# Optimization experiments

Hardware: AMD Instinct MI355X
Metric: run time of the kernel (lower is better)

Reference implementation:

```python
import jax, jax.numpy as jnp
import numpy as np

DIM = 384
HEADS = 12
WS = 7
HID = 4 * 256  # FFN hidden is hard-coded default 1024, NOT 4*dim
EPS = 1e-5


def layernorm(x, g, b):
    mu = jnp.mean(x, axis=-1, keepdims=True)
    var = jnp.mean(jnp.square(x - mu), axis=-1, keepdims=True)
    return (x - mu) * jax.lax.rsqrt(var + EPS) * g + b


def setup_inputs() -> dict:
    key = jax.random.key(0)
    ks = jax.random.split(key, 12)
    s = 0.02
    return {
        "x": jax.random.normal(ks[0], (32, DIM, 56, 56), dtype=jnp.float32),
        "ln1_g": jnp.ones((DIM,), jnp.float32),
        "ln1_b": jnp.zeros((DIM,), jnp.float32),
        "qkv_w": jax.random.normal(ks[1], (3 * DIM, DIM), jnp.float32) * s,
        "qkv_b": jnp.zeros((3 * DIM,), jnp.float32),
        "proj_w": jax.random.normal(ks[2], (DIM, DIM), jnp.float32) * s,
        "proj_b": jnp.zeros((DIM,), jnp.float32),
        "ln2_g": jnp.ones((DIM,), jnp.float32),
        "ln2_b": jnp.zeros((DIM,), jnp.float32),
        "fc1_w": jax.random.normal(ks[3], (HID, DIM), jnp.float32) * s,
        "fc1_b": jnp.zeros((HID,), jnp.float32),
        "fc2_w": jax.random.normal(ks[4], (DIM, HID), jnp.float32) * s,
        "fc2_b": jnp.zeros((DIM,), jnp.float32),
    }


def window_attention(x, qkv_w, qkv_b, proj_w, proj_b):
    # x: [B, H, W, C] channels-last
    B, H, W, C = x.shape
    Wh, Ww = H // WS, W // WS
    # partition: [B*Wh*Ww, WS*WS, C]
    w = x.reshape(B, Wh, WS, Ww, WS, C).transpose(0, 1, 3, 2, 4, 5)
    w = w.reshape(B * Wh * Ww, WS * WS, C)
    Bn, N, _ = w.shape
    hd = C // HEADS
    qkv = w @ qkv_w.T + qkv_b  # [Bn, N, 3C]
    qkv = qkv.reshape(Bn, N, 3, HEADS, hd).transpose(2, 0, 3, 1, 4)
    q, k, v = qkv[0], qkv[1], qkv[2]  # each [Bn, h, N, hd]
    attn = jnp.einsum('bhnd,bhmd->bhnm', q, k) * (hd ** -0.5)
    attn = jax.nn.softmax(attn, axis=-1)
    o = jnp.einsum('bhnm,bhmd->bhnd', attn, v)
    o = o.transpose(0, 2, 1, 3).reshape(Bn, N, C)
    o = o @ proj_w.T + proj_b
    # reverse
    o = o.reshape(B, Wh, Ww, WS, WS, C).transpose(0, 1, 3, 2, 4, 5)
    return o.reshape(B, H, W, C)


def reference(x, ln1_g, ln1_b, qkv_w, qkv_b, proj_w, proj_b,
              ln2_g, ln2_b, fc1_w, fc1_b, fc2_w, fc2_b):
    # x: [B, C, H, W]
    residual = x
    h = x.transpose(0, 2, 3, 1)  # [B,H,W,C]
    h = layernorm(h, ln1_g, ln1_b)
    h = window_attention(h, qkv_w, qkv_b, proj_w, proj_b)
    x = h.transpose(0, 3, 1, 2) + residual
    residual = x
    h = x.transpose(0, 2, 3, 1)
    h = layernorm(h, ln2_g, ln2_b)
    h = jax.nn.gelu(h @ fc1_w.T + fc1_b, approximate=False)
    h = h @ fc2_w.T + fc2_b
    return h.transpose(0, 3, 1, 2) + residual
```

## Files before the change

### kernel.cpp

```cpp
#include <hip/hip_runtime.h>
#include <cstdint>
#include <cmath>

#define DIM 384
#define HEADS 12
#define TOKENS 100352
#define HW_ 3136
#define NWIN 2048

typedef __attribute__((ext_vector_type(8))) short short8;
typedef __attribute__((ext_vector_type(4))) short short4v;
typedef __attribute__((ext_vector_type(2))) short short2v;
typedef __attribute__((ext_vector_type(4))) float f32x4;

#define AS1 __attribute__((address_space(1)))
#define AS3 __attribute__((address_space(3)))

__device__ __forceinline__ short f2b(float f){
  unsigned u = __builtin_bit_cast(unsigned, f);
  u += 0x7FFFu + ((u >> 16) & 1u);
  return (short)(u >> 16);
}
__device__ __forceinline__ float b2f(short h){
  unsigned u = ((unsigned)(unsigned short)h) << 16;
  return __builtin_bit_cast(float, u);
}

__device__ __forceinline__ void gload_lds16(const short* g, short* l){
  __builtin_amdgcn_global_load_lds((AS1 void*)(g), (AS3 void*)(l), 16, 0, 0);
}

__device__ __forceinline__ float gelu_f(float v){
  float z  = v * 0.70710678118654752f;
  float az = fabsf(z);
  float t  = __builtin_amdgcn_rcpf(1.f + 0.3275911f*az);
  float poly = t*(0.254829592f + t*(-0.284496736f + t*(1.421413741f +
               t*(-1.453152027f + t*1.061405429f))));
  float e  = __expf(-z*z);
  float er = copysignf(1.f - poly*e, z);
  return 0.5f * v * (1.f + er);
}

__global__ void k_cvt(const float* __restrict__ s, short* __restrict__ d, int n){
  int i = blockIdx.x*256 + threadIdx.x;
  if (i < n) d[i] = f2b(s[i]);
}

__global__ __launch_bounds__(256) void k_ln1(const float* __restrict__ x,
    const float* __restrict__ gam, const float* __restrict__ bet,
    short* __restrict__ ln1, short* __restrict__ xr)
{
  __shared__ float red0[256];
  __shared__ float red1[256];
  __shared__ float mus[64], rss[64];
  __shared__ short xfull[64*388];
  int t = threadIdx.x;
  int blk = blockIdx.x;
  int b = blk / 49;
  int hw0 = (blk % 49) * 64;
  int p = t & 63, cq = t >> 6;
  const float* xb = x + (long)b*DIM*HW_ + hw0 + p;
  float s = 0.f, sq = 0.f;
  for (int i = 0; i < 96; i++){
    int c = i*4 + cq;
    float v = xb[(long)c*HW_];
    s += v; sq += v*v;
    xfull[p*388 + c] = f2b(v);
  }
  red0[t] = s; red1[t] = sq;
  __syncthreads();
  if (t < 64){
    float ts = red0[t] + red0[t+64] + red0[t+128] + red0[t+192];
    float tq = red1[t] + red1[t+64] + red1[t+128] + red1[t+192];
    float mu = ts * (1.f/DIM);
    float var = tq * (1.f/DIM) - mu*mu;
    mus[t] = mu;
    rss[t] = rsqrtf(var + 1e-5f);
  }
  __syncthreads();
  int p2 = t >> 2, q4 = t & 3;
  float mu = mus[p2], rs = rss[p2];
  int hwp2 = hw0 + p2;
  int h2 = hwp2 / 56, w2 = hwp2 % 56;
  int wt2 = ((b*8 + h2/7)*8 + w2/7)*49 + (h2%7)*7 + (w2%7);
  long lnbase = (long)wt2*DIM;
  long xrbase = (long)(b*HW_ + hwp2)*DIM;
  #pragma unroll
  for (int cc0 = 0; cc0 < DIM; cc0 += 32){
    short8 xv = *(const short8*)(xfull + p2*388 + cc0 + q4*8);
    short8 lv;
    #pragma unroll
    for (int u = 0; u < 8; u++){
      int c = cc0 + q4*8 + u;
      float v = b2f(xv[u]);
      lv[u] = f2b((v - mu)*rs*gam[c] + bet[c]);
    }
    *(short8*)(ln1 + lnbase + cc0 + q4*8) = lv;
    *(short8*)(xr + xrbase + cc0 + q4*8) = xv;
  }
}

#define EPI_BIAS 0
#define EPI_PROJ 1
#define EPI_GELU 2
#define EPI_OUT  4

template<int EPI>
__global__ __launch_bounds__(256) void k_gemm(
    const short* __restrict__ A, const short* __restrict__ B,
    const float* __restrict__ bias, short* __restrict__ out,
    const short* __restrict__ res, int M, int N, int K, int ntiles)
{
  constexpr int ES = (EPI == EPI_OUT) ? 133 : 132;
  __shared__ short sm[20480];
  float* E = (float*)sm;

  int nwg = gridDim.x;
  int orig = blockIdx.x;
  int bid = (orig & 7) * (nwg >> 3) + (orig >> 3);
  int nt = bid % ntiles, mt = bid / ntiles;
  int m0 = mt*128, n0 = nt*128;
  int t = threadIdx.x;
  int lane = t & 63, wv = t >> 6;
  int wm = wv >> 1, wn = wv & 1;
  int gg = lane >> 4, cc = lane & 15;

  int srow = t >> 2;
  int skc = ((t & 3) ^ (srow & 3)) << 3;
  const short* Ab = A + (long)(m0 + srow)*K + skc;
  const short* Bb = B + (long)(n0 + srow)*K + skc;
  long rowstep = 64L*K;

  int goff = (gg << 3) ^ ((cc & 3) << 3);

  f32x4 acc[4][4];
  #pragma unroll
  for (int i=0;i<4;i++)
    #pragma unroll
    for (int j=0;j<4;j++) acc[i][j] = (f32x4){0.f,0.f,0.f,0.f};

  int nk = K >> 5;

  gload_lds16(Ab,           sm + t*8);
  gload_lds16(Ab + rowstep, sm + (t+256)*8);
  gload_lds16(Bb,           sm + 12288 + t*8);
  gload_lds16(Bb + rowstep, sm + 12288 + (t+256)*8);
  gload_lds16(Ab + 32,           sm + 4096 + t*8);
  gload_lds16(Ab + 32 + rowstep, sm + 4096 + (t+256)*8);

  int ac = 0, bc = 0;
  for (int kt = 0; kt < nk; kt++){
    if (kt + 1 < nk) { asm volatile("s_waitcnt vmcnt(2) lgkmcnt(0)" ::: "memory"); }
    else             { asm volatile("s_waitcnt vmcnt(0) lgkmcnt(0)" ::: "memory"); }
    __builtin_amdgcn_s_barrier();
    if (kt + 1 < nk){
      long ko = (long)(kt+1) << 5;
      int bn = bc ^ 1;
      gload_lds16(Bb + ko,           sm + 12288 + bn*4096 + t*8);
      gload_lds16(Bb + ko + rowstep, sm + 12288 + bn*4096 + (t+256)*8);
    }
    if (kt + 2 < nk){
      long ko = (long)(kt+2) << 5;
      int an = ac + 2; if (an >= 3) an -= 3;
      gload_lds16(Ab + ko,           sm + an*4096 + t*8);
      gload_lds16(Ab + ko + rowstep, sm + an*4096 + (t+256)*8);
    }
    const short* Ac = sm + ac*4096;
    const short* Bc = sm + 12288 + bc*4096;
    short8 af[4], bfv[4];
    #pragma unroll
    for (int mi=0;mi<4;mi++) af[mi] = *(const short8*)(Ac + (wm*64 + mi*16 + cc)*32 + goff);
    #pragma unroll
    for (int ni=0;ni<4;ni++) bfv[ni] = *(const short8*)(Bc + (wn*64 + ni*16 + cc)*32 + goff);
    #pragma unroll
    for (int mi=0;mi<4;mi++)
      #pragma unroll
      for (int ni=0;ni<4;ni++)
        acc[mi][ni] = __builtin_amdgcn_mfma_f32_16x16x32_bf16(af[mi], bfv[ni], acc[mi][ni], 0, 0, 0);
    ac = (ac + 1 == 3) ? 0 : ac + 1;
    bc ^= 1;
  }

  if constexpr (EPI == EPI_OUT) {
    float* outf = (float*)out;
    #pragma unroll
    for (int p = 0; p < 2; p++){
      __syncthreads();
      if (wm == p){
        #pragma unroll
        for (int mi=0;mi<4;mi++){
          #pragma unroll
          for (int r=0;r<4;r++){
            float* Er = E + (mi*16 + gg*4 + r)*ES + wn*64 + cc;
            Er[0]  = acc[mi][0][r];
            Er[16] = acc[mi][1][r];
            Er[32] = acc[mi][2][r];
            Er[48] = acc[mi][3][r];
          }
        }
      }
      __syncthreads();
      #pragma unroll
      for (int jj = 0; jj < 8; jj++){
        int unit = jj*256 + t;
        int crow = unit >> 5, chunk = unit & 31;
        int row = m0 + p*64 + crow;
        f32x4 v = *(const f32x4*)(E + crow*ES + chunk*4);
        f32x4 bv = *(const f32x4*)(bias + n0 + chunk*4);
        short4v rv = *(const short4v*)(res + (long)row*N + n0 + chunk*4);
        #pragma unroll
        for (int j = 0; j < 4; j++) v[j] += bv[j] + b2f(rv[j]);
        *(f32x4*)(E + crow*ES + chunk*4) = v;
      }
      __syncthreads();
      #pragma unroll
      for (int jj = 0; jj < 32; jj++){
        int unit = jj*256 + t;
        int c = unit >> 6, rl = unit & 63;
        int token = m0 + p*64 + rl;
        int b = token / HW_;
        int hw = token - b*HW_;
        outf[((long)b*DIM + n0 + c)*HW_ + hw] = E[rl*ES + c];
      }
    }
  } else {
    #pragma unroll
    for (int p = 0; p < 2; p++){
      __syncthreads();
      #pragma unroll
      for (int mh = 0; mh < 2; mh++){
        #pragma unroll
        for (int r = 0; r < 4; r++){
          int crow = wm*32 + mh*16 + gg*4 + r;
          float* Er = E + crow*ES + wn*64 + cc;
          Er[0]  = acc[mh*2 + p][0][r];
          Er[16] = acc[mh*2 + p][1][r];
          Er[32] = acc[mh*2 + p][2][r];
          Er[48] = acc[mh*2 + p][3][r];
        }
      }
      __syncthreads();
      #pragma unroll
      for (int jj = 0; jj < 8; jj++){
        int unit = jj*256 + t;
        int crow = unit >> 5, chunk = unit & 31;
        int rr = crow & 15, mh = (crow >> 4) & 1, wmr = crow >> 5;
        int row = m0 + wmr*64 + (mh*2 + p)*16 + rr;
        int col = n0 + chunk*4;
        f32x4 v = *(const f32x4*)(E + crow*ES + chunk*4);
        f32x4 bv = *(const f32x4*)(bias + col);
        long orow;
        if constexpr (EPI == EPI_PROJ) {
          int b = row / HW_; int rem = row % HW_;
          int wid = rem / 49, idx = rem % 49;
          int hh = (wid >> 3)*7 + idx/7;
          int ww = (wid & 7)*7 + idx%7;
          orow = (long)(b*HW_ + hh*56 + ww)*N;
        } else {
          orow = (long)row*N;
        }
        float vv[4];
        #pragma unroll
        for (int j = 0; j < 4; j++){
          vv[j] = v[j] + bv[j];
          if constexpr (EPI == EPI_GELU) vv[j] = gelu_f(vv[j]);
        }
        if constexpr (EPI == EPI_PROJ){
          short4v rv = *(const short4v*)(res + orow + col);
          #pragma unroll
          for (int j = 0; j < 4; j++) vv[j] += b2f(rv[j]);
        }
        short4v ov;
        #pragma unroll
        for (int j = 0; j < 4; j++) ov[j] = f2b(vv[j]);
        *(short4v*)(out + orow + col) = ov;
      }
    }
  }
}

__global__ __launch_bounds__(256) void k_ln2(const short* __restrict__ x2,
  const float* __restrict__ gam, const float* __restrict__ bet, short* __restrict__ o)
{
  int t = threadIdx.x, lane = t & 63, wv = t >> 6;
  long row = (long)blockIdx.x*4 + wv;
  const short* xr = x2 + row*DIM;
  short4v a = *(const short4v*)(xr + lane*4);
  short2v b2 = *(const short2v*)(xr + 256 + lane*2);
  float f[6] = {b2f(a[0]),b2f(a[1]),b2f(a[2]),b2f(a[3]),b2f(b2[0]),b2f(b2[1])};
  float s = 0.f, sq = 0.f;
  #pragma unroll
  for (int i=0;i<6;i++){ s += f[i]; sq += f[i]*f[i]; }
  #pragma unroll
  for (int off=1; off<64; off<<=1){ s += __shfl_xor(s, off); sq += __shfl_xor(sq, off); }
  float mu = s*(1.f/DIM);
  float var = sq*(1.f/DIM) - mu*mu;
  float rs = rsqrtf(var + 1e-5f);
  int c0 = lane*4, c1 = 256 + lane*2;
  short4v oa; short2v ob;
  #pragma unroll
  for (int i=0;i<4;i++) oa[i] = f2b((f[i]-mu)*rs*gam[c0+i] + bet[c0+i]);
  #pragma unroll
  for (int j=0;j<2;j++) ob[j] = f2b((f[4+j]-mu)*rs*gam[c1+j] + bet[c1+j]);
  *(short4v*)(o + row*DIM + c0) = oa;
  *(short2v*)(o + row*DIM + c1) = ob;
}

__global__ __launch_bounds__(256) void k_attn(const short* __restrict__ qkv, short* __restrict__ o)
{
  __shared__ short lds[4*7424];
  int t = threadIdx.x;
  int lane = t & 63, wv = t >> 6;
  int w = blockIdx.x;
  int h = wv + (int)blockIdx.y*4;
  short* Qs = lds + wv*7424;
  short* Ks = Qs + 2560;
  short* Vt = Ks + 2560;
  short* Pl = Qs;
  int g = lane >> 4, c = lane & 15;
  int nrow = lane >> 2;
  int dc = (lane & 3) * 8;
  const float scale = 0.17677669529663687f;

  long base = (long)w*49*1152 + h*32;
  #pragma unroll
  for (int it = 0; it < 4; it++){
    int n = it*16 + nrow;
    short8 vq = {0,0,0,0,0,0,0,0};
    short8 vk = vq, vvv = vq;
    if (n < 49){
      vq  = *(const short8*)(qkv + base + (long)n*1152 + dc);
      vk  = *(const short8*)(qkv + base + (long)n*1152 + 384 + dc);
      vvv = *(const short8*)(qkv + base + (long)n*1152 + 768 + dc);
    }
    *(short8*)(Qs + n*40 + dc) = vq;
    *(short8*)(Ks + n*40 + dc) = vk;
    #pragma unroll
    for (int u = 0; u < 8; u++) Vt[(dc+u)*72 + n] = vvv[u];
  }
  asm volatile("s_waitcnt lgkmcnt(0)" ::: "memory");
  __builtin_amdgcn_sched_barrier(0);

  f32x4 sacc[4][4];
  #pragma unroll
  for (int i=0;i<4;i++)
    #pragma unroll
    for (int j=0;j<4;j++) sacc[i][j] = (f32x4){0.f,0.f,0.f,0.f};
  short8 kf[4];
  #pragma unroll
  for (int ni=0;ni<4;ni++) kf[ni] = *(const short8*)(Ks + (ni*16 + c)*40 + g*8);
  #pragma unroll
  for (int mi=0;mi<4;mi++){
    short8 a = *(const short8*)(Qs + (mi*16 + c)*40 + g*8);
    #pragma unroll
    for (int ni=0;ni<4;ni++)
      sacc[mi][ni] = __builtin_amdgcn_mfma_f32_16x16x32_bf16(a, kf[ni], sacc[mi][ni], 0, 0, 0);
  }
  #pragma unroll
  for (int mi=0;mi<4;mi++){
    #pragma unroll
    for (int r=0;r<4;r++){
      float v0 = sacc[mi][0][r]*scale;
      float v1 = sacc[mi][1][r]*scale;
      float v2 = sacc[mi][2][r]*scale;
      float v3 = (c >= 1) ? -1e30f : sacc[mi][3][r]*scale;
      float mx = fmaxf(fmaxf(v0,v1), fmaxf(v2,v3));
      #pragma unroll
      for (int off=1; off<16; off<<=1) mx = fmaxf(mx, __shfl_xor(mx, off));
      float e0 = __expf(v0-mx), e1 = __expf(v1-mx), e2 = __expf(v2-mx), e3 = __expf(v3-mx);
      float sm = e0+e1+e2+e3;
      #pragma unroll
      for (int off=1; off<16; off<<=1) sm += __shfl_xor(sm, off);
      float inv = 1.f/sm;
      int prow = mi*16 + g*4 + r;
      Pl[prow*72 +      c] = f2b(e0*inv);
      Pl[prow*72 + 16 + c] = f2b(e1*inv);
      Pl[prow*72 + 32 + c] = f2b(e2*inv);
      Pl[prow*72 + 48 + c] = f2b(e3*inv);
    }
  }
  asm volatile("s_waitcnt lgkmcnt(0)" ::: "memory");
  __builtin_amdgcn_sched_barrier(0);

  f32x4 oacc[4][2];
  #pragma unroll
  for (int i=0;i<4;i++){ oacc[i][0] = (f32x4){0.f,0.f,0.f,0.f}; oacc[i][1] = oacc[i][0]; }
  #pragma unroll
  for (int ks=0; ks<2; ks++){
    short8 bb0 = *(const short8*)(Vt + (c)*72      + ks*32 + g*8);
    short8 bb1 = *(const short8*)(Vt + (16 + c)*72 + ks*32 + g*8);
    #pragma unroll
    for (int mi=0;mi<4;mi++){
      short8 aa = *(const short8*)(Pl + (mi*16 + c)*72 + ks*32 + g*8);
      oacc[mi][0] = __builtin_amdgcn_mfma_f32_16x16x32_bf16(aa, bb0, oacc[mi][0], 0, 0, 0);
      oacc[mi][1] = __builtin_amdgcn_mfma_f32_16x16x32_bf16(aa, bb1, oacc[mi][1], 0, 0, 0);
    }
  }
  #pragma unroll
  for (int mi=0;mi<4;mi++){
    #pragma unroll
    for (int r=0;r<4;r++){
      int row = mi*16 + g*4 + r;
      if (row < 49){
        long ob = ((long)w*49 + row)*384 + h*32;
        o[ob + c]      = f2b(oacc[mi][0][r]);
        o[ob + 16 + c] = f2b(oacc[mi][1][r]);
      }
    }
  }
}

extern "C" void kernel_launch(void* const* d_in, const int* in_sizes, int n_in,
                              void* d_out, int out_size, void* d_ws, size_t ws_size,
                              hipStream_t stream) {
  (void)in_sizes; (void)n_in; (void)out_size; (void)ws_size;
  const float* x      = (const float*)d_in[0];
  const float* ln1_g  = (const float*)d_in[1];
  const float* ln1_b  = (const float*)d_in[2];
  const float* qkv_w  = (const float*)d_in[3];
  const float* qkv_b  = (const float*)d_in[4];
  const float* proj_w = (const float*)d_in[5];
  const float* proj_b = (const float*)d_in[6];
  const float* ln2_g  = (const float*)d_in[7];
  const float* ln2_b  = (const float*)d_in[8];
  const float* fc1_w  = (const float*)d_in[9];
  const float* fc1_b  = (const float*)d_in[10];
  const float* fc2_w  = (const float*)d_in[11];
  const float* fc2_b  = (const float*)d_in[12];

  char* ws = (char*)d_ws;
  short* buf1 = (short*)(ws);
  short* buf2 = (short*)(ws + 231211008L);
  short* buf3 = (short*)(ws + 308281344L);
  short* buf4 = (short*)(ws + 385351680L);
  short* buf5 = (short*)(ws + 462422016L);
  short* wq = (short*)(ws + 539492352L);
  short* wp = wq + 442368;
  short* w1 = wp + 147456;
  short* w2 = w1 + 393216;

  k_cvt<<<dim3((442368+255)/256), dim3(256), 0, stream>>>(qkv_w, wq, 442368);
  k_cvt<<<dim3((147456+255)/256), dim3(256), 0, stream>>>(proj_w, wp, 147456);
  k_cvt<<<dim3((393216+255)/256), dim3(256), 0, stream>>>(fc1_w, w1, 393216);
  k_cvt<<<dim3((393216+255)/256), dim3(256), 0, stream>>>(fc2_w, w2, 393216);

  k_ln1<<<dim3(1568), dim3(256), 0, stream>>>(x, ln1_g, ln1_b, buf2, buf5);

  k_gemm<EPI_BIAS><<<dim3(784*9), dim3(256), 0, stream>>>(buf2, wq, qkv_b, buf1, nullptr,
                                                          TOKENS, 1152, 384, 9);
  k_attn<<<dim3(NWIN, 3), dim3(256), 0, stream>>>(buf1, buf3);

  k_gemm<EPI_PROJ><<<dim3(784*3), dim3(256), 0, stream>>>(buf3, wp, proj_b, buf4, buf5,
                                                          TOKENS, 384, 384, 3);
  k_ln2<<<dim3(TOKENS/4), dim3(256), 0, stream>>>(buf4, ln2_g, ln2_b, buf2);

  k_gemm<EPI_GELU><<<dim3(784*8), dim3(256), 0, stream>>>(buf2, w1, fc1_b, buf1, nullptr,
                                                          TOKENS, 1024, 384, 8);
  k_gemm<EPI_OUT><<<dim3(784*3), dim3(256), 0, stream>>>(buf1, w2, fc2_b, (short*)d_out, buf4,
                                                         TOKENS, 384, 1024, 3);
}
```

Baseline: 720.5 us.

## Add 256x256-tile 8-wave pipelined GEMM for FC1 with GELU epilogue

Adds a new bf16 MFMA GEMM kernel with 256x256 output tiles, 512 threads, double-buffered LDS filled by direct global-to-LDS loads, interleaved half-tile loads and MFMA phases, and a workgroup remap across XCDs. FC1+GELU now uses this kernel instead of the generic 128-ish tile GEMM. The aim is more operand reuse per tile and overlap of global loads with matrix math. The cost is 128KB of LDS per block, which limits occupancy to one block per CU, plus a staged epilogue through LDS.

```diff
diff --git a/kernel.cpp b/kernel.cpp
--- a/kernel.cpp
+++ b/kernel.cpp
@@ -279,6 +279,173 @@
   }
 }
 
+template<int K>
+__global__ __launch_bounds__(512) void k_gemm8(
+    const short* __restrict__ A, const short* __restrict__ B,
+    const float* __restrict__ bias, short* __restrict__ out,
+    int M, int N, int ntiles)
+{
+  __shared__ short sm8[65536];
+  float* E = (float*)sm8;
+
+  constexpr int NT = K >> 6;
+
+  int nwg = gridDim.x;
+  int orig = blockIdx.x;
+  int bid = (orig & 7) * (nwg >> 3) + (orig >> 3);
+  int ntb = bid % ntiles, mt = bid / ntiles;
+  int m0 = mt*256, n0 = ntb*256;
+  int t = threadIdx.x;
+  int lane = t & 63, wv = t >> 6;
+  int wr = wv >> 2, wc = wv & 3;
+  int cc = lane & 15, gg = lane >> 4;
+
+  int srow = t >> 2;
+  int schunk = (t & 3) ^ ((t >> 3) & 3);
+  const short* Asrc = A + (long)(m0 + srow)*K + schunk*8;
+  const short* Bsrc = B + (long)(n0 + srow)*K + schunk*8;
+  const long rstep = 128L*K;
+
+  int sw = (gg ^ ((cc >> 1) & 3)) * 8;
+  int aoff = (wr*128 + cc)*32 + sw;
+  int boff = (wc*64  + cc)*32 + sw;
+
+  f32x4 acc[8][4];
+  #pragma unroll
+  for (int i=0;i<8;i++)
+    #pragma unroll
+    for (int j=0;j<4;j++) acc[i][j] = (f32x4){0.f,0.f,0.f,0.f};
+
+  gload_lds16(Asrc,                 sm8 + t*8);
+  gload_lds16(Asrc + rstep,         sm8 + (t+512)*8);
+  gload_lds16(Bsrc,                 sm8 + 16384 + t*8);
+  gload_lds16(Bsrc + rstep,         sm8 + 16384 + (t+512)*8);
+  gload_lds16(Asrc + 32,            sm8 + 8192 + t*8);
+  gload_lds16(Asrc + 32 + rstep,    sm8 + 8192 + (t+512)*8);
+  gload_lds16(Bsrc + 32,            sm8 + 16384 + 8192 + t*8);
+  gload_lds16(Bsrc + 32 + rstep,    sm8 + 16384 + 8192 + (t+512)*8);
+  asm volatile("s_waitcnt vmcnt(0)" ::: "memory");
+  __syncthreads();
+
+  #pragma unroll
+  for (int tau = 0; tau < NT; tau++){
+    const int cur = tau & 1, nb = cur ^ 1;
+    const short* Ac = sm8 + cur*32768;
+    const short* Bc = Ac + 16384;
+    short* And = sm8 + nb*32768;
+    short* Bnd = And + 16384;
+    const long ko = (long)(tau+1)*64;
+    short8 af[4], bf[4];
+
+    if (tau + 1 < NT){
+      gload_lds16(Asrc + ko,         And + t*8);
+      gload_lds16(Asrc + ko + rstep, And + (t+512)*8);
+    }
+    #pragma unroll
+    for (int i=0;i<4;i++) af[i] = *(const short8*)(Ac + i*512 + aoff);
+    #pragma unroll
+    for (int i=0;i<4;i++) bf[i] = *(const short8*)(Bc + i*512 + boff);
+    asm volatile("s_waitcnt lgkmcnt(0)" ::: "memory");
+    __builtin_amdgcn_s_barrier();
+    __builtin_amdgcn_sched_barrier(0);
+    __builtin_amdgcn_s_setprio(1);
+    #pragma unroll
+    for (int i=0;i<4;i++)
+      #pragma unroll
+      for (int j=0;j<4;j++)
+        acc[i][j] = __builtin_amdgcn_mfma_f32_16x16x32_bf16(af[i], bf[j], acc[i][j], 0, 0, 0);
+    __builtin_amdgcn_s_setprio(0);
+    __builtin_amdgcn_s_barrier();
+
+    if (tau + 1 < NT){
+      gload_lds16(Bsrc + ko,         Bnd + t*8);
+      gload_lds16(Bsrc + ko + rstep, Bnd + (t+512)*8);
+    }
+    #pragma unroll
+    for (int i=0;i<4;i++) af[i] = *(const short8*)(Ac + 2048 + i*512 + aoff);
+    if (tau == NT-1) { asm volatile("s_waitcnt vmcnt(0) lgkmcnt(0)" ::: "memory"); }
+    else             { asm volatile("s_waitcnt vmcnt(4) lgkmcnt(0)" ::: "memory"); }
+    __builtin_amdgcn_s_barrier();
+    __builtin_amdgcn_sched_barrier(0);
+    __builtin_amdgcn_s_setprio(1);
+    #pragma unroll
+    for (int i=0;i<4;i++)
+      #pragma unroll
+      for (int j=0;j<4;j++)
+        acc[4+i][j] = __builtin_amdgcn_mfma_f32_16x16x32_bf16(af[i], bf[j], acc[4+i][j], 0, 0, 0);
+    __builtin_amdgcn_s_setprio(0);
+    __builtin_amdgcn_s_barrier();
+
+    if (tau + 1 < NT){
+      gload_lds16(Asrc + ko + 32,         And + 8192 + t*8);
+      gload_lds16(Asrc + ko + 32 + rstep, And + 8192 + (t+512)*8);
+    }
+    #pragma unroll
+    for (int i=0;i<4;i++) af[i] = *(const short8*)(Ac + 8192 + i*512 + aoff);
+    #pragma unroll
+    for (int i=0;i<4;i++) bf[i] = *(const short8*)(Bc + 8192 + i*512 + boff);
+    asm volatile("s_waitcnt lgkmcnt(0)" ::: "memory");
+    __builtin_amdgcn_s_barrier();
+    __builtin_amdgcn_sched_barrier(0);
+    __builtin_amdgcn_s_setprio(1);
+    #pragma unroll
+    for (int i=0;i<4;i++)
+      #pragma unroll
+      for (int j=0;j<4;j++)
+        acc[i][j] = __builtin_amdgcn_mfma_f32_16x16x32_bf16(af[i], bf[j], acc[i][j], 0, 0, 0);
+    __builtin_amdgcn_s_setprio(0);
+    __builtin_amdgcn_s_barrier();
+
+    if (tau + 1 < NT){
+      gload_lds16(Bsrc + ko + 32,         Bnd + 8192 + t*8);
+      gload_lds16(Bsrc + ko + 32 + rstep, Bnd + 8192 + (t+512)*8);
+    }
+    #pragma unroll
+    for (int i=0;i<4;i++) af[i] = *(const short8*)(Ac + 8192 + 2048 + i*512 + aoff);
+    if (tau < NT-1) { asm volatile("s_waitcnt vmcnt(4) lgkmcnt(0)" ::: "memory"); }
+    else            { asm volatile("s_waitcnt lgkmcnt(0)" ::: "memory"); }
+    __builtin_amdgcn_s_barrier();
+    __builtin_amdgcn_sched_barrier(0);
+    __builtin_amdgcn_s_setprio(1);
+    #pragma unroll
+    for (int i=0;i<4;i++)
+      #pragma unroll
+      for (int j=0;j<4;j++)
+        acc[4+i][j] = __builtin_amdgcn_mfma_f32_16x16x32_bf16(af[i], bf[j], acc[4+i][j], 0, 0, 0);
+    __builtin_amdgcn_s_setprio(0);
+    __builtin_amdgcn_s_barrier();
+  }
+
+  #pragma unroll
+  for (int pp = 0; pp < 4; pp++){
+    __syncthreads();
+    if (wr == (pp >> 1)){
+      int mh = pp & 1;
+      #pragma unroll
+      for (int mi2=0; mi2<4; mi2++){
+        #pragma unroll
+        for (int ni=0; ni<4; ni++){
+          #pragma unroll
+          for (int r=0; r<4; r++)
+            E[(mi2*16 + gg*4 + r)*260 + wc*64 + ni*16 + cc] = acc[mh*4+mi2][ni][r];
+        }
+      }
+    }
+    __syncthreads();
+    #pragma unroll
+    for (int jj = 0; jj < 8; jj++){
+      int unit = jj*512 + t;
+      int crow = unit >> 6, chunk = unit & 63;
+      f32x4 v = *(const f32x4*)(E + crow*260 + chunk*4);
+      f32x4 bv = *(const f32x4*)(bias + n0 + chunk*4);
+      short4v ov;
+      #pragma unroll
+      for (int j=0;j<4;j++) ov[j] = f2b(gelu_f(v[j] + bv[j]));
+      *(short4v*)(out + (long)(m0 + pp*64 + crow)*N + n0 + chunk*4) = ov;
+    }
+  }
+}
+
 __global__ __launch_bounds__(256) void k_ln2(const short* __restrict__ x2,
   const float* __restrict__ gam, const float* __restrict__ bet, short* __restrict__ o)
 {
@@ -454,8 +621,8 @@
                                                           TOKENS, 384, 384, 3);
   k_ln2<<<dim3(TOKENS/4), dim3(256), 0, stream>>>(buf4, ln2_g, ln2_b, buf2);
 
-  k_gemm<EPI_GELU><<<dim3(784*8), dim3(256), 0, stream>>>(buf2, w1, fc1_b, buf1, nullptr,
-                                                          TOKENS, 1024, 384, 8);
+  k_gemm8<384><<<dim3(392*4), dim3(512), 0, stream>>>(buf2, w1, fc1_b, buf1,
+                                                      TOKENS, 1024, 4);
   k_gemm<EPI_OUT><<<dim3(784*3), dim3(256), 0, stream>>>(buf1, w2, fc2_b, (short*)d_out, buf4,
                                                          TOKENS, 384, 1024, 3);
 }
```

Result: slower. 747.0 us (+3.7%).
